# Performance work log

Hardware: AMD Instinct MI355X
Metric: run time of the kernel (lower is better)

Reference implementation:

```python
import jax, jax.numpy as jnp
import numpy as np

H = 256  # hidden size for both encoder and decoder

def gru_cell(x, h, Wih, Whh, bih, bhh):
    # PyTorch nn.GRU cell: gates ordered (r, z, n)
    gi = x @ Wih.T + bih            # [N, 3H]
    gh = h @ Whh.T + bhh            # [N, 3H]
    ir, iz, inn = jnp.split(gi, 3, axis=-1)
    hr, hz, hn = jnp.split(gh, 3, axis=-1)
    r = jax.nn.sigmoid(ir + hr)
    z = jax.nn.sigmoid(iz + hz)
    n = jnp.tanh(inn + r * hn)
    return (1.0 - z) * n + z * h


def setup_inputs() -> dict:
    key = jax.random.key(0)
    ks = jax.random.split(key, 16)
    s = 0.05
    inp = {
        'x': jax.random.normal(ks[0], (32768, 15, 4), jnp.float32),
        'enc_embed_W': jax.random.normal(ks[1], (H, 4), jnp.float32) * s,
        'enc_embed_b': jax.random.normal(ks[2], (H,), jnp.float32) * s,
        'enc_Wih': jax.random.normal(ks[3], (3 * H, H), jnp.float32) * s,
        'enc_Whh': jax.random.normal(ks[4], (3 * H, H), jnp.float32) * s,
        'enc_bih': jax.random.normal(ks[5], (3 * H,), jnp.float32) * s,
        'enc_bhh': jax.random.normal(ks[6], (3 * H,), jnp.float32) * s,
        'dec_embed_W': jax.random.normal(ks[7], (H, H), jnp.float32) * s,
        'dec_embed_b': jax.random.normal(ks[8], (H,), jnp.float32) * s,
        'dec_Wih': jax.random.normal(ks[9], (3 * H, H), jnp.float32) * s,
        'dec_Whh': jax.random.normal(ks[10], (3 * H, H), jnp.float32) * s,
        'dec_bih': jax.random.normal(ks[11], (3 * H,), jnp.float32) * s,
        'dec_bhh': jax.random.normal(ks[12], (3 * H,), jnp.float32) * s,
        'out_W': jax.random.normal(ks[13], (4, H), jnp.float32) * s,
        'out_b': jax.random.normal(ks[14], (4,), jnp.float32) * s,
        'pred_len': 45,
    }
    return inp


def reference(x, enc_embed_W, enc_embed_b, enc_Wih, enc_Whh, enc_bih, enc_bhh,
              dec_embed_W, dec_embed_b, dec_Wih, dec_Whh, dec_bih, dec_bhh,
              out_W, out_b, pred_len):
    N = x.shape[0]
    # enc_embed: Linear + ReLU
    traj_feats = jax.nn.relu(jnp.einsum('nti,hi->nth', x, enc_embed_W) + enc_embed_b)
    # Encoder GRU over time (batch_first); we only need the final hidden state.
    h0 = jnp.zeros((N, H), x.dtype)

    def enc_step(h, xt):
        h = gru_cell(xt, h, enc_Wih, enc_Whh, enc_bih, enc_bhh)
        return h, None

    h_enc, _ = jax.lax.scan(enc_step, h0, jnp.swapaxes(traj_feats, 0, 1))

    dec_in0 = jax.nn.relu(h_enc @ dec_embed_W.T + dec_embed_b)

    def dec_step(carry, _):
        h, dec_in = carry
        h = gru_cell(dec_in, h, dec_Wih, dec_Whh, dec_bih, dec_bhh)
        out_t = h @ out_W.T + out_b                     # [N, 4]
        dec_in = jax.nn.relu(h @ dec_embed_W.T + dec_embed_b)
        return (h, dec_in), out_t

    _, outs = jax.lax.scan(dec_step, (h_enc, dec_in0), None, length=pred_len)
    return jnp.swapaxes(outs, 0, 1)  # [N, pred_len, 4]
```

## Files before the change

kernel.cpp:

```cpp
#include <hip/hip_runtime.h>
#include <hip/hip_fp16.h>

#define HD    256
#define TENC  15
#define PLEN  45
#define MROW  128
#define NTHR  512
#define NBLK  (32768 / MROW)

typedef __attribute__((ext_vector_type(16))) float     f32x16;
typedef __attribute__((ext_vector_type(8)))  _Float16  f16x8;

#define MFMAH __builtin_amdgcn_mfma_f32_32x32x16_f16

__device__ __forceinline__ float fast_sig(float x) {
    float e = __builtin_amdgcn_exp2f(-1.44269504088896f * x);
    return __builtin_amdgcn_rcpf(1.f + e);
}
__device__ __forceinline__ float fast_tanh(float x) {
    float e = __builtin_amdgcn_exp2f(-2.88539008177793f * x);
    return (1.f - e) * __builtin_amdgcn_rcpf(1.f + e);
}

__global__ void xpose_w_kernel(const float* __restrict__ src,
                               _Float16* __restrict__ dst, int n_gcols) {
    int t = blockIdx.x * blockDim.x + threadIdx.x;
    if (t >= n_gcols * 32) return;
    int gcol = t >> 5, c8 = t & 31;
    int kk = c8 >> 1, hi = c8 & 1;
    const float* s = src + (size_t)gcol * HD + c8 * 8;
    int seg = gcol >> 8, gc = gcol & 255;
    size_t d = (size_t)seg * 65536 +
               ((size_t)(((gc >> 5) * 16 + kk) * 64 + hi * 32 + (gc & 31))) * 8;
    _Float16 v[8];
    #pragma unroll
    for (int e = 0; e < 8; ++e) v[e] = (_Float16)s[e];
    *(f16x8*)(dst + d) = *(f16x8*)v;
}

__global__ void xpose_ow_kernel(const float* __restrict__ src,
                                _Float16* __restrict__ dst) {
    int t = blockIdx.x * blockDim.x + threadIdx.x;
    if (t >= 32 * 32) return;
    int gcol = t >> 5, c8 = t & 31;
    int kk = c8 >> 1, hi = c8 & 1;
    _Float16 v[8];
    if (gcol < 4) {
        const float* s = src + (size_t)gcol * HD + c8 * 8;
        #pragma unroll
        for (int e = 0; e < 8; ++e) v[e] = (_Float16)s[e];
    } else {
        #pragma unroll
        for (int e = 0; e < 8; ++e) v[e] = (_Float16)0.f;
    }
    size_t d = ((size_t)(kk * 64 + hi * 32 + gcol)) * 8;
    *(f16x8*)(dst + d) = *(f16x8*)v;
}

__device__ __forceinline__ int swz(int row, int col) {
    return row * 512 + ((((col >> 3) ^ row) & 31) << 4) + ((col & 7) << 1);
}

__global__ __launch_bounds__(NTHR, 2) void gru_main(
    const float* __restrict__ x,
    const float* __restrict__ eW, const float* __restrict__ eb,
    const _Float16* __restrict__ encWih, const _Float16* __restrict__ encWhh,
    const float* __restrict__ enc_bih, const float* __restrict__ enc_bhh,
    const _Float16* __restrict__ decEW, const float* __restrict__ dec_eb,
    const _Float16* __restrict__ decWih, const _Float16* __restrict__ decWhh,
    const float* __restrict__ dec_bih, const float* __restrict__ dec_bhh,
    const _Float16* __restrict__ outWt, const float* __restrict__ outb,
    float* __restrict__ out)
{
    __shared__ __align__(16) char ls_a[MROW * 512];
    __shared__ __align__(16) char ls_h[MROW * 512];
    __shared__ float ls_ew[HD * 4];
    __shared__ float ls_eb[HD];
    __shared__ float ls_bias[4 * HD];
    __shared__ float ls_deb[HD];

    const int tid   = threadIdx.x;
    const int lane  = tid & 63;
    const int wv    = tid >> 6;
    const int rowA  = lane & 31;
    const int hi    = lane >> 5;
    const int col   = wv * 32 + rowA;
    const int nbase = blockIdx.x * MROW;

    for (int i = tid; i < HD * 4; i += NTHR) ls_ew[i] = eW[i];
    if (tid < HD) {
        ls_eb[tid]            = eb[tid];
        ls_bias[tid]          = enc_bih[tid] + enc_bhh[tid];
        ls_bias[HD + tid]     = enc_bih[HD + tid] + enc_bhh[HD + tid];
        ls_bias[2 * HD + tid] = enc_bih[2 * HD + tid];
        ls_bias[3 * HD + tid] = enc_bhh[2 * HD + tid];
    }
    for (int i = tid; i < MROW * 512 / 4; i += NTHR) ((unsigned int*)ls_h)[i] = 0u;

    float bR, bZ, bN, bH;
    float deb, bb;

    f32x16 accA[4], accB[4];

    const char* pa = ls_a + rowA * 512;
    const char* ph = ls_h + rowA * 512;

    auto bcast = [](float v) {
        f32x16 a;
        #pragma unroll
        for (int i = 0; i < 16; ++i) a[i] = v;
        return a;
    };

    auto pass1 = [&](const _Float16* Wi, const _Float16* Wh) {
        #pragma unroll
        for (int rt = 0; rt < 4; ++rt) { accA[rt] = bcast(bR); accB[rt] = bcast(bH); }
        const _Float16* bi = Wi + wv * 8192 + lane * 8;
        const _Float16* bh = Wh + wv * 8192 + lane * 8;
        #pragma unroll 2
        for (int kk = 0; kk < 16; ++kk) {
            const int sh = (((kk * 2 + hi) ^ rowA) & 31) << 4;
            f16x8 bri = *(const f16x8*)(bi + kk * 512);
            f16x8 brh = *(const f16x8*)(bh + kk * 512);
            f16x8 bnh = *(const f16x8*)(bh + kk * 512 + 131072);
            #pragma unroll
            for (int rt = 0; rt < 4; ++rt) {
                f16x8 ax = *(const f16x8*)(pa + rt * 16384 + sh);
                f16x8 ah = *(const f16x8*)(ph + rt * 16384 + sh);
                accA[rt] = MFMAH(ax, bri, accA[rt], 0, 0, 0);
                accA[rt] = MFMAH(ah, brh, accA[rt], 0, 0, 0);
                accB[rt] = MFMAH(ah, bnh, accB[rt], 0, 0, 0);
            }
        }
    };

    auto mid = [&]() {
        #pragma unroll
        for (int rt = 0; rt < 4; ++rt)
            #pragma unroll
            for (int q = 0; q < 16; ++q)
                accB[rt][q] = fmaf(fast_sig(accA[rt][q]), accB[rt][q], bN);
    };

    auto pass2 = [&](const _Float16* Wi, const _Float16* Wh) {
        #pragma unroll
        for (int rt = 0; rt < 4; ++rt) accA[rt] = bcast(bZ);
        const _Float16* bi = Wi + wv * 8192 + lane * 8;
        const _Float16* bh = Wh + wv * 8192 + lane * 8;
        #pragma unroll 2
        for (int kk = 0; kk < 16; ++kk) {
            const int sh = (((kk * 2 + hi) ^ rowA) & 31) << 4;
            f16x8 bzi = *(const f16x8*)(bi + kk * 512 + 65536);
            f16x8 bzh = *(const f16x8*)(bh + kk * 512 + 65536);
            f16x8 bni = *(const f16x8*)(bi + kk * 512 + 131072);
            #pragma unroll
            for (int rt = 0; rt < 4; ++rt) {
                f16x8 ax = *(const f16x8*)(pa + rt * 16384 + sh);
                f16x8 ah = *(const f16x8*)(ph + rt * 16384 + sh);
                accA[rt] = MFMAH(ax, bzi, accA[rt], 0, 0, 0);
                accA[rt] = MFMAH(ah, bzh, accA[rt], 0, 0, 0);
                accB[rt] = MFMAH(ax, bni, accB[rt], 0, 0, 0);
            }
        }
    };

    auto final_write = [&]() {
        #pragma unroll
        for (int rt = 0; rt < 4; ++rt)
            #pragma unroll
            for (int q = 0; q < 16; ++q) {
                int row = rt * 32 + (q & 3) + ((q >> 2) << 3) + (hi << 2);
                _Float16* p = (_Float16*)(ls_h + swz(row, col));
                float ho = (float)*p;
                float z = fast_sig(accA[rt][q]);
                float n = fast_tanh(accB[rt][q]);
                *p = (_Float16)fmaf(z, ho - n, n);
            }
    };

    auto embed_step = [&](int t) {
        int row = tid & 127;
        int c0  = (tid >> 7) * 64;
        const float4 xv = *(const float4*)(x + ((size_t)(nbase + row) * TENC + t) * 4);
        #pragma unroll 8
        for (int j = 0; j < 64; ++j) {
            int c = c0 + j;
            const float* wp = &ls_ew[c * 4];
            float v = fmaf(xv.x, wp[0], fmaf(xv.y, wp[1],
                      fmaf(xv.z, wp[2], fmaf(xv.w, wp[3], ls_eb[c]))));
            *(_Float16*)(ls_a + swz(row, c)) = (_Float16)fmaxf(v, 0.f);
        }
    };

    auto dec_embed = [&]() {
        f32x16 o0 = bcast(deb), o1 = o0, o2 = o0, o3 = o0;
        const _Float16* be = decEW + wv * 8192 + lane * 8;
        #pragma unroll 2
        for (int kk = 0; kk < 16; ++kk) {
            const int sh = (((kk * 2 + hi) ^ rowA) & 31) << 4;
            f16x8 b = *(const f16x8*)(be + kk * 512);
            o0 = MFMAH(*(const f16x8*)(ph + sh),          b, o0, 0, 0, 0);
            o1 = MFMAH(*(const f16x8*)(ph + 16384 + sh),  b, o1, 0, 0, 0);
            o2 = MFMAH(*(const f16x8*)(ph + 32768 + sh),  b, o2, 0, 0, 0);
            o3 = MFMAH(*(const f16x8*)(ph + 49152 + sh),  b, o3, 0, 0, 0);
        }
        #pragma unroll
        for (int rt = 0; rt < 4; ++rt) {
            const f32x16& o = rt == 0 ? o0 : rt == 1 ? o1 : rt == 2 ? o2 : o3;
            #pragma unroll
            for (int q = 0; q < 16; ++q) {
                int row = rt * 32 + (q & 3) + ((q >> 2) << 3) + (hi << 2);
                *(_Float16*)(ls_a + swz(row, col)) = (_Float16)fmaxf(o[q], 0.f);
            }
        }
    };

    auto out_layer = [&](int t) {
        if ((wv & 1) == 0) {
            const int rt = wv >> 1;
            f32x16 o = bcast(bb);
            const char* pH = ph + rt * 16384;
            const _Float16* bo = outWt + lane * 8;
            #pragma unroll 2
            for (int kk = 0; kk < 16; ++kk) {
                const int sh = (((kk * 2 + hi) ^ rowA) & 31) << 4;
                f16x8 a = *(const f16x8*)(pH + sh);
                f16x8 b = *(const f16x8*)(bo + kk * 512);
                o = MFMAH(a, b, o, 0, 0, 0);
            }
            if (rowA < 4) {
                #pragma unroll
                for (int q = 0; q < 16; ++q) {
                    int row = rt * 32 + (q & 3) + ((q >> 2) << 3) + (hi << 2);
                    out[((size_t)(nbase + row) * PLEN + t) * 4 + rowA] = o[q];
                }
            }
        }
    };

    __syncthreads();
    bR = ls_bias[col];
    bZ = ls_bias[HD + col];
    bN = ls_bias[2 * HD + col];
    bH = ls_bias[3 * HD + col];
    embed_step(0);
    __syncthreads();

    for (int t = 0; t < TENC; ++t) {
        pass1(encWih, encWhh);
        mid();
        pass2(encWih, encWhh);
        __syncthreads();
        final_write();
        if (t + 1 < TENC) embed_step(t + 1);
        __syncthreads();
    }

    if (tid < HD) {
        ls_bias[tid]          = dec_bih[tid] + dec_bhh[tid];
        ls_bias[HD + tid]     = dec_bih[HD + tid] + dec_bhh[HD + tid];
        ls_bias[2 * HD + tid] = dec_bih[2 * HD + tid];
        ls_bias[3 * HD + tid] = dec_bhh[2 * HD + tid];
        ls_deb[tid]           = dec_eb[tid];
    }
    __syncthreads();
    bR = ls_bias[col];
    bZ = ls_bias[HD + col];
    bN = ls_bias[2 * HD + col];
    bH = ls_bias[3 * HD + col];
    deb = ls_deb[col];
    bb  = (rowA < 4) ? outb[rowA] : 0.f;
    dec_embed();
    __syncthreads();

    for (int t = 0; t < PLEN; ++t) {
        pass1(decWih, decWhh);
        mid();
        pass2(decWih, decWhh);
        __syncthreads();
        final_write();
        __syncthreads();
        dec_embed();
        __syncthreads();
        out_layer(t);
    }
}

extern "C" void kernel_launch(void* const* d_in, const int* in_sizes, int n_in,
                              void* d_out, int out_size, void* d_ws, size_t ws_size,
                              hipStream_t stream) {
    const float* x       = (const float*)d_in[0];
    const float* eW      = (const float*)d_in[1];
    const float* eb      = (const float*)d_in[2];
    const float* encWihf = (const float*)d_in[3];
    const float* encWhhf = (const float*)d_in[4];
    const float* enc_bih = (const float*)d_in[5];
    const float* enc_bhh = (const float*)d_in[6];
    const float* decEWf  = (const float*)d_in[7];
    const float* dec_eb  = (const float*)d_in[8];
    const float* decWihf = (const float*)d_in[9];
    const float* decWhhf = (const float*)d_in[10];
    const float* dec_bih = (const float*)d_in[11];
    const float* dec_bhh = (const float*)d_in[12];
    const float* outW    = (const float*)d_in[13];
    const float* outb    = (const float*)d_in[14];

    _Float16* ws = (_Float16*)d_ws;
    _Float16* hWih_e = ws;
    _Float16* hWhh_e = ws + 196608;
    _Float16* hWih_d = ws + 2 * 196608;
    _Float16* hWhh_d = ws + 3 * 196608;
    _Float16* hEW_d  = ws + 4 * 196608;
    _Float16* hOWt   = ws + 4 * 196608 + 65536;

    const int t1 = 768 * 32;
    const int t2 = 256 * 32;
    xpose_w_kernel<<<(t1 + 255) / 256, 256, 0, stream>>>(encWihf, hWih_e, 768);
    xpose_w_kernel<<<(t1 + 255) / 256, 256, 0, stream>>>(encWhhf, hWhh_e, 768);
    xpose_w_kernel<<<(t1 + 255) / 256, 256, 0, stream>>>(decWihf, hWih_d, 768);
    xpose_w_kernel<<<(t1 + 255) / 256, 256, 0, stream>>>(decWhhf, hWhh_d, 768);
    xpose_w_kernel<<<(t2 + 255) / 256, 256, 0, stream>>>(decEWf,  hEW_d,  256);
    xpose_ow_kernel<<<4, 256, 0, stream>>>(outW, hOWt);

    gru_main<<<NBLK, NTHR, 0, stream>>>(
        x, eW, eb, hWih_e, hWhh_e, enc_bih, enc_bhh,
        hEW_d, dec_eb, hWih_d, hWhh_d, dec_bih, dec_bhh,
        hOWt, outb, (float*)d_out);
}
```

Measured before the change: 2.427 ms.

## Shrink block tile to 32 rows with 4 waves each owning 64 columns

Measured after the change: 4.086 ms. +68.4%, slower.

```diff
diff --git a/kernel.cpp b/kernel.cpp
--- a/kernel.cpp
+++ b/kernel.cpp
@@ -4,8 +4,8 @@
 #define HD    256
 #define TENC  15
 #define PLEN  45
-#define MROW  128
-#define NTHR  512
+#define MROW  32
+#define NTHR  256
 #define NBLK  (32768 / MROW)
 
 typedef __attribute__((ext_vector_type(16))) float     f32x16;
@@ -61,7 +61,7 @@
     return row * 512 + ((((col >> 3) ^ row) & 31) << 4) + ((col & 7) << 1);
 }
 
-__global__ __launch_bounds__(NTHR, 2) void gru_main(
+__global__ __launch_bounds__(NTHR, 3) void gru_main(
     const float* __restrict__ x,
     const float* __restrict__ eW, const float* __restrict__ eb,
     const _Float16* __restrict__ encWih, const _Float16* __restrict__ encWhh,
@@ -84,7 +84,8 @@
     const int wv    = tid >> 6;
     const int rowA  = lane & 31;
     const int hi    = lane >> 5;
-    const int col   = wv * 32 + rowA;
+    const int col0  = wv * 64 + rowA;
+    const int col1  = wv * 64 + 32 + rowA;
     const int nbase = blockIdx.x * MROW;
 
     for (int i = tid; i < HD * 4; i += NTHR) ls_ew[i] = eW[i];
@@ -97,10 +98,10 @@
     }
     for (int i = tid; i < MROW * 512 / 4; i += NTHR) ((unsigned int*)ls_h)[i] = 0u;
 
-    float bR, bZ, bN, bH;
-    float deb, bb;
-
-    f32x16 accA[4], accB[4];
+    float bR0, bR1, bZ0, bZ1, bN0, bN1, bH0, bH1;
+    float deb0, deb1, bb;
+
+    f32x16 accA[2], accB[2];
 
     const char* pa = ls_a + rowA * 512;
     const char* ph = ls_h + rowA * 512;
@@ -113,77 +114,84 @@
     };
 
     auto pass1 = [&](const _Float16* Wi, const _Float16* Wh) {
-        #pragma unroll
-        for (int rt = 0; rt < 4; ++rt) { accA[rt] = bcast(bR); accB[rt] = bcast(bH); }
-        const _Float16* bi = Wi + wv * 8192 + lane * 8;
-        const _Float16* bh = Wh + wv * 8192 + lane * 8;
+        accA[0] = bcast(bR0); accA[1] = bcast(bR1);
+        accB[0] = bcast(bH0); accB[1] = bcast(bH1);
+        const _Float16* bi0 = Wi + (2 * wv) * 8192 + lane * 8;
+        const _Float16* bh0 = Wh + (2 * wv) * 8192 + lane * 8;
         #pragma unroll 2
         for (int kk = 0; kk < 16; ++kk) {
             const int sh = (((kk * 2 + hi) ^ rowA) & 31) << 4;
-            f16x8 bri = *(const f16x8*)(bi + kk * 512);
-            f16x8 brh = *(const f16x8*)(bh + kk * 512);
-            f16x8 bnh = *(const f16x8*)(bh + kk * 512 + 131072);
-            #pragma unroll
-            for (int rt = 0; rt < 4; ++rt) {
-                f16x8 ax = *(const f16x8*)(pa + rt * 16384 + sh);
-                f16x8 ah = *(const f16x8*)(ph + rt * 16384 + sh);
-                accA[rt] = MFMAH(ax, bri, accA[rt], 0, 0, 0);
-                accA[rt] = MFMAH(ah, brh, accA[rt], 0, 0, 0);
-                accB[rt] = MFMAH(ah, bnh, accB[rt], 0, 0, 0);
-            }
+            f16x8 ax = *(const f16x8*)(pa + sh);
+            f16x8 ah = *(const f16x8*)(ph + sh);
+            f16x8 b0 = *(const f16x8*)(bi0 + kk * 512);
+            f16x8 b1 = *(const f16x8*)(bi0 + kk * 512 + 8192);
+            accA[0] = MFMAH(ax, b0, accA[0], 0, 0, 0);
+            accA[1] = MFMAH(ax, b1, accA[1], 0, 0, 0);
+            b0 = *(const f16x8*)(bh0 + kk * 512);
+            b1 = *(const f16x8*)(bh0 + kk * 512 + 8192);
+            accA[0] = MFMAH(ah, b0, accA[0], 0, 0, 0);
+            accA[1] = MFMAH(ah, b1, accA[1], 0, 0, 0);
+            b0 = *(const f16x8*)(bh0 + kk * 512 + 131072);
+            b1 = *(const f16x8*)(bh0 + kk * 512 + 131072 + 8192);
+            accB[0] = MFMAH(ah, b0, accB[0], 0, 0, 0);
+            accB[1] = MFMAH(ah, b1, accB[1], 0, 0, 0);
         }
     };
 
     auto mid = [&]() {
         #pragma unroll
-        for (int rt = 0; rt < 4; ++rt)
-            #pragma unroll
-            for (int q = 0; q < 16; ++q)
-                accB[rt][q] = fmaf(fast_sig(accA[rt][q]), accB[rt][q], bN);
+        for (int q = 0; q < 16; ++q) {
+            accB[0][q] = fmaf(fast_sig(accA[0][q]), accB[0][q], bN0);
+            accB[1][q] = fmaf(fast_sig(accA[1][q]), accB[1][q], bN1);
+        }
     };
 
     auto pass2 = [&](const _Float16* Wi, const _Float16* Wh) {
-        #pragma unroll
-        for (int rt = 0; rt < 4; ++rt) accA[rt] = bcast(bZ);
-        const _Float16* bi = Wi + wv * 8192 + lane * 8;
-        const _Float16* bh = Wh + wv * 8192 + lane * 8;
+        accA[0] = bcast(bZ0); accA[1] = bcast(bZ1);
+        const _Float16* bi0 = Wi + (2 * wv) * 8192 + lane * 8;
+        const _Float16* bh0 = Wh + (2 * wv) * 8192 + lane * 8;
         #pragma unroll 2
         for (int kk = 0; kk < 16; ++kk) {
             const int sh = (((kk * 2 + hi) ^ rowA) & 31) << 4;
-            f16x8 bzi = *(const f16x8*)(bi + kk * 512 + 65536);
-            f16x8 bzh = *(const f16x8*)(bh + kk * 512 + 65536);
-            f16x8 bni = *(const f16x8*)(bi + kk * 512 + 131072);
-            #pragma unroll
-            for (int rt = 0; rt < 4; ++rt) {
-                f16x8 ax = *(const f16x8*)(pa + rt * 16384 + sh);
-                f16x8 ah = *(const f16x8*)(ph + rt * 16384 + sh);
-                accA[rt] = MFMAH(ax, bzi, accA[rt], 0, 0, 0);
-                accA[rt] = MFMAH(ah, bzh, accA[rt], 0, 0, 0);
-                accB[rt] = MFMAH(ax, bni, accB[rt], 0, 0, 0);
-            }
+            f16x8 ax = *(const f16x8*)(pa + sh);
+            f16x8 ah = *(const f16x8*)(ph + sh);
+            f16x8 b0 = *(const f16x8*)(bi0 + kk * 512 + 65536);
+            f16x8 b1 = *(const f16x8*)(bi0 + kk * 512 + 65536 + 8192);
+            accA[0] = MFMAH(ax, b0, accA[0], 0, 0, 0);
+            accA[1] = MFMAH(ax, b1, accA[1], 0, 0, 0);
+            b0 = *(const f16x8*)(bh0 + kk * 512 + 65536);
+            b1 = *(const f16x8*)(bh0 + kk * 512 + 65536 + 8192);
+            accA[0] = MFMAH(ah, b0, accA[0], 0, 0, 0);
+            accA[1] = MFMAH(ah, b1, accA[1], 0, 0, 0);
+            b0 = *(const f16x8*)(bi0 + kk * 512 + 131072);
+            b1 = *(const f16x8*)(bi0 + kk * 512 + 131072 + 8192);
+            accB[0] = MFMAH(ax, b0, accB[0], 0, 0, 0);
+            accB[1] = MFMAH(ax, b1, accB[1], 0, 0, 0);
         }
     };
 
     auto final_write = [&]() {
         #pragma unroll
-        for (int rt = 0; rt < 4; ++rt)
-            #pragma unroll
-            for (int q = 0; q < 16; ++q) {
-                int row = rt * 32 + (q & 3) + ((q >> 2) << 3) + (hi << 2);
-                _Float16* p = (_Float16*)(ls_h + swz(row, col));
-                float ho = (float)*p;
-                float z = fast_sig(accA[rt][q]);
-                float n = fast_tanh(accB[rt][q]);
-                *p = (_Float16)fmaf(z, ho - n, n);
-            }
+        for (int q = 0; q < 16; ++q) {
+            int row = (q & 3) + ((q >> 2) << 3) + (hi << 2);
+            _Float16* p0 = (_Float16*)(ls_h + swz(row, col0));
+            _Float16* p1 = (_Float16*)(ls_h + swz(row, col1));
+            float h0 = (float)*p0, h1 = (float)*p1;
+            float z0 = fast_sig(accA[0][q]);
+            float n0 = fast_tanh(accB[0][q]);
+            float z1 = fast_sig(accA[1][q]);
+            float n1 = fast_tanh(accB[1][q]);
+            *p0 = (_Float16)fmaf(z0, h0 - n0, n0);
+            *p1 = (_Float16)fmaf(z1, h1 - n1, n1);
+        }
     };
 
     auto embed_step = [&](int t) {
-        int row = tid & 127;
-        int c0  = (tid >> 7) * 64;
+        int row = tid & 31;
+        int c0  = (tid >> 5) * 32;
         const float4 xv = *(const float4*)(x + ((size_t)(nbase + row) * TENC + t) * 4);
         #pragma unroll 8
-        for (int j = 0; j < 64; ++j) {
+        for (int j = 0; j < 32; ++j) {
             int c = c0 + j;
             const float* wp = &ls_ew[c * 4];
             float v = fmaf(xv.x, wp[0], fmaf(xv.y, wp[1],
@@ -193,45 +201,40 @@
     };
 
     auto dec_embed = [&]() {
-        f32x16 o0 = bcast(deb), o1 = o0, o2 = o0, o3 = o0;
-        const _Float16* be = decEW + wv * 8192 + lane * 8;
+        f32x16 o0 = bcast(deb0), o1 = bcast(deb1);
+        const _Float16* be = decEW + (2 * wv) * 8192 + lane * 8;
         #pragma unroll 2
         for (int kk = 0; kk < 16; ++kk) {
             const int sh = (((kk * 2 + hi) ^ rowA) & 31) << 4;
-            f16x8 b = *(const f16x8*)(be + kk * 512);
-            o0 = MFMAH(*(const f16x8*)(ph + sh),          b, o0, 0, 0, 0);
-            o1 = MFMAH(*(const f16x8*)(ph + 16384 + sh),  b, o1, 0, 0, 0);
-            o2 = MFMAH(*(const f16x8*)(ph + 32768 + sh),  b, o2, 0, 0, 0);
-            o3 = MFMAH(*(const f16x8*)(ph + 49152 + sh),  b, o3, 0, 0, 0);
-        }
-        #pragma unroll
-        for (int rt = 0; rt < 4; ++rt) {
-            const f32x16& o = rt == 0 ? o0 : rt == 1 ? o1 : rt == 2 ? o2 : o3;
-            #pragma unroll
-            for (int q = 0; q < 16; ++q) {
-                int row = rt * 32 + (q & 3) + ((q >> 2) << 3) + (hi << 2);
-                *(_Float16*)(ls_a + swz(row, col)) = (_Float16)fmaxf(o[q], 0.f);
-            }
+            f16x8 a = *(const f16x8*)(ph + sh);
+            f16x8 b0 = *(const f16x8*)(be + kk * 512);
+            f16x8 b1 = *(const f16x8*)(be + kk * 512 + 8192);
+            o0 = MFMAH(a, b0, o0, 0, 0, 0);
+            o1 = MFMAH(a, b1, o1, 0, 0, 0);
+        }
+        #pragma unroll
+        for (int q = 0; q < 16; ++q) {
+            int row = (q & 3) + ((q >> 2) << 3) + (hi << 2);
+            *(_Float16*)(ls_a + swz(row, col0)) = (_Float16)fmaxf(o0[q], 0.f);
+            *(_Float16*)(ls_a + swz(row, col1)) = (_Float16)fmaxf(o1[q], 0.f);
         }
     };
 
     auto out_layer = [&](int t) {
-        if ((wv & 1) == 0) {
-            const int rt = wv >> 1;
+        if (wv == 0) {
             f32x16 o = bcast(bb);
-            const char* pH = ph + rt * 16384;
             const _Float16* bo = outWt + lane * 8;
             #pragma unroll 2
             for (int kk = 0; kk < 16; ++kk) {
                 const int sh = (((kk * 2 + hi) ^ rowA) & 31) << 4;
-                f16x8 a = *(const f16x8*)(pH + sh);
+                f16x8 a = *(const f16x8*)(ph + sh);
                 f16x8 b = *(const f16x8*)(bo + kk * 512);
                 o = MFMAH(a, b, o, 0, 0, 0);
             }
             if (rowA < 4) {
                 #pragma unroll
                 for (int q = 0; q < 16; ++q) {
-                    int row = rt * 32 + (q & 3) + ((q >> 2) << 3) + (hi << 2);
+                    int row = (q & 3) + ((q >> 2) << 3) + (hi << 2);
                     out[((size_t)(nbase + row) * PLEN + t) * 4 + rowA] = o[q];
                 }
             }
@@ -239,10 +242,10 @@
     };
 
     __syncthreads();
-    bR = ls_bias[col];
-    bZ = ls_bias[HD + col];
-    bN = ls_bias[2 * HD + col];
-    bH = ls_bias[3 * HD + col];
+    bR0 = ls_bias[col0];          bR1 = ls_bias[col1];
+    bZ0 = ls_bias[HD + col0];     bZ1 = ls_bias[HD + col1];
+    bN0 = ls_bias[2 * HD + col0]; bN1 = ls_bias[2 * HD + col1];
+    bH0 = ls_bias[3 * HD + col0]; bH1 = ls_bias[3 * HD + col1];
     embed_step(0);
     __syncthreads();
 
@@ -264,12 +267,12 @@
         ls_deb[tid]           = dec_eb[tid];
     }
     __syncthreads();
-    bR = ls_bias[col];
-    bZ = ls_bias[HD + col];
-    bN = ls_bias[2 * HD + col];
-    bH = ls_bias[3 * HD + col];
-    deb = ls_deb[col];
-    bb  = (rowA < 4) ? outb[rowA] : 0.f;
+    bR0 = ls_bias[col0];          bR1 = ls_bias[col1];
+    bZ0 = ls_bias[HD + col0];     bZ1 = ls_bias[HD + col1];
+    bN0 = ls_bias[2 * HD + col0]; bN1 = ls_bias[2 * HD + col1];
+    bH0 = ls_bias[3 * HD + col0]; bH1 = ls_bias[3 * HD + col1];
+    deb0 = ls_deb[col0];          deb1 = ls_deb[col1];
+    bb   = (rowA < 4) ? outb[rowA] : 0.f;
     dec_embed();
     __syncthreads();
 
```
